# Optimization experiments

Hardware: AMD Instinct MI355X
Metric: run time of the kernel (lower is better)

The kernel has to match this reference:

```python
import jax, jax.numpy as jnp
import numpy as np

N_NODES = 100000
NEG_SLOPE = 0.2


def _gat_layer(x, src, dst, W, a_src, a_dst, b):
    """Single-head PyG-style GATConv (heads=1, concat, self-loops already in src/dst)."""
    h = x @ W                                   # [N, out]
    alpha_s = h @ a_src                          # [N]
    alpha_d = h @ a_dst                          # [N]
    e = jax.nn.leaky_relu(alpha_s[src] + alpha_d[dst], NEG_SLOPE)  # [E]
    # numerically stable softmax over incoming edges of each dst node
    m = jax.ops.segment_max(e, dst, num_segments=N_NODES)           # [N]
    ex = jnp.exp(e - m[dst])                                        # [E]
    denom = jax.ops.segment_sum(ex, dst, num_segments=N_NODES)      # [N]
    attn = ex / denom[dst]                                          # [E]
    out = jax.ops.segment_sum(h[src] * attn[:, None], dst, num_segments=N_NODES)
    return out + b


def setup_inputs() -> dict:
    key = jax.random.key(0)
    ks = jax.random.split(key, 16)
    F_IN, H1, H2 = 256, 64, 32
    E = 1600000
    x = jax.random.normal(ks[0], (N_NODES, F_IN), dtype=jnp.float32)
    edge_index = jax.random.randint(ks[1], (2, E), 0, N_NODES, dtype=jnp.int32)
    def glorot(k, shape):
        lim = float(np.sqrt(6.0 / (shape[0] + shape[-1])))
        return jax.random.uniform(k, shape, jnp.float32, -lim, lim)
    return {
        "x": x,
        "edge_index": edge_index,
        "W1": glorot(ks[2], (F_IN, H1)),
        "a_src1": glorot(ks[3], (H1,)),
        "a_dst1": glorot(ks[4], (H1,)),
        "b1": jnp.zeros((H1,), jnp.float32),
        "W2": glorot(ks[5], (H1, H2)),
        "a_src2": glorot(ks[6], (H2,)),
        "a_dst2": glorot(ks[7], (H2,)),
        "b2": jnp.zeros((H2,), jnp.float32),
        "Wfc": glorot(ks[8], (H2, 1)),
        "bfc": jnp.zeros((1,), jnp.float32),
    }


def reference(x, edge_index, W1, a_src1, a_dst1, b1, W2, a_src2, a_dst2, b2, Wfc, bfc):
    # add self loops (PyG GATConv default add_self_loops=True)
    loop = jnp.arange(N_NODES, dtype=edge_index.dtype)
    src = jnp.concatenate([edge_index[0], loop])
    dst = jnp.concatenate([edge_index[1], loop])
    h = jax.nn.relu(_gat_layer(x, src, dst, W1, a_src1, a_dst1, b1))
    h = jax.nn.relu(_gat_layer(h, src, dst, W2, a_src2, a_dst2, b2))
    return h @ Wfc + bfc  # [N, 1]
```

## Files before the change

kernel.cpp:

```cpp
#include <hip/hip_runtime.h>
#include <hip/hip_bf16.h>

#define NEG_SLOPE 0.2f
#define NINF (-1e30f)

#define BKT_BITS 7
#define BKT 128
#define PB 256

typedef __attribute__((ext_vector_type(8))) short s8v;
typedef __attribute__((ext_vector_type(4))) float f4v;

__device__ __forceinline__ unsigned short f2bf(float f) {
    unsigned u = __float_as_uint(f);
    u = (u + 0x7fffu + ((u >> 16) & 1u)) >> 16;
    return (unsigned short)u;
}
__device__ __forceinline__ float bf2f(unsigned short h) {
    return __uint_as_float(((unsigned)h) << 16);
}


__global__ __launch_bounds__(256) void hist_pb_k(
    const int* __restrict__ edst, int E, int Etot, int NBK, int EPB,
    int* __restrict__ counts)
{
    __shared__ int lh[1024];
    for (int i = threadIdx.x; i < NBK; i += 256) lh[i] = 0;
    __syncthreads();
    const int e0 = blockIdx.x * EPB;
    const int e1 = min(e0 + EPB, Etot);
    for (int i = e0 + threadIdx.x; i < e1; i += 256) {
        int d = (i < E) ? edst[i] : (i - E);
        atomicAdd(&lh[d >> BKT_BITS], 1);
    }
    __syncthreads();
    for (int b = threadIdx.x; b < NBK; b += 256)
        counts[b * PB + blockIdx.x] = lh[b];
}

__global__ __launch_bounds__(256) void scan_partial_k(
    const int* __restrict__ a, int L, int* __restrict__ partials)
{
    __shared__ int red[256];
    const int t = threadIdx.x;
    const int base = blockIdx.x * 1024 + t * 4;
    int sum = 0;
    #pragma unroll
    for (int k = 0; k < 4; ++k) {
        int i = base + k;
        if (i < L) sum += a[i];
    }
    red[t] = sum;
    __syncthreads();
    #pragma unroll
    for (int o = 128; o; o >>= 1) {
        if (t < o) red[t] += red[t + o];
        __syncthreads();
    }
    if (t == 0) partials[blockIdx.x] = red[0];
}

__global__ __launch_bounds__(256) void scan_partials_k(
    int* __restrict__ partials, int nb)
{
    __shared__ int sh[256];
    const int t = threadIdx.x;
    int v = (t < nb) ? partials[t] : 0;
    sh[t] = v;
    __syncthreads();
    #pragma unroll
    for (int o = 1; o < 256; o <<= 1) {
        int u = (t >= o) ? sh[t - o] : 0;
        __syncthreads();
        sh[t] += u;
        __syncthreads();
    }
    if (t < nb) partials[t] = sh[t] - v;
}

__global__ __launch_bounds__(256) void scan_final_k(
    int* __restrict__ a, const int* __restrict__ partials, int L)
{
    __shared__ int sh[256];
    const int t = threadIdx.x;
    const int base = blockIdx.x * 1024 + t * 4;
    int v[4];
    int sum = 0;
    #pragma unroll
    for (int k = 0; k < 4; ++k) {
        int i = base + k;
        v[k] = (i < L) ? a[i] : 0;
        sum += v[k];
    }
    sh[t] = sum;
    __syncthreads();
    #pragma unroll
    for (int o = 1; o < 256; o <<= 1) {
        int u = (t >= o) ? sh[t - o] : 0;
        __syncthreads();
        sh[t] += u;
        __syncthreads();
    }
    int run = sh[t] - sum + partials[blockIdx.x];
    #pragma unroll
    for (int k = 0; k < 4; ++k) {
        int i = base + k;
        if (i < L) a[i] = run;
        run += v[k];
    }
}

__global__ __launch_bounds__(256) void scatter_pb_k(
    const int* __restrict__ esrc, const int* __restrict__ edst,
    int E, int Etot, int NBK, int EPB,
    const int* __restrict__ cbase, unsigned* __restrict__ tmp)
{
    __shared__ int cur[1024];
    for (int b = threadIdx.x; b < NBK; b += 256)
        cur[b] = cbase[b * PB + blockIdx.x];
    __syncthreads();
    const int e0 = blockIdx.x * EPB;
    const int e1 = min(e0 + EPB, Etot);
    for (int i = e0 + threadIdx.x; i < e1; i += 256) {
        int d = (i < E) ? edst[i] : (i - E);
        int s = (i < E) ? esrc[i] : (i - E);
        int pos = atomicAdd(&cur[d >> BKT_BITS], 1);
        tmp[pos] = ((unsigned)s << BKT_BITS) | (unsigned)(d & (BKT - 1));
    }
}

__global__ __launch_bounds__(256) void bucket_finalize_k(
    const unsigned* __restrict__ tmp, const int* __restrict__ cbase,
    int N, int NBK, int Etot,
    int* __restrict__ rowptr, int* __restrict__ csr)
{
    __shared__ int cnt[BKT];
    __shared__ int off[BKT];
    const int b = blockIdx.x;
    const int t = threadIdx.x;
    const int start = cbase[b * PB];
    const int end = (b + 1 < NBK) ? cbase[(b + 1) * PB] : Etot;
    const int n0 = b << BKT_BITS;
    const int nn = min(BKT, N - n0);

    if (t < BKT) cnt[t] = 0;
    __syncthreads();
    for (int i = start + t; i < end; i += 256)
        atomicAdd(&cnt[tmp[i] & (BKT - 1)], 1);
    __syncthreads();
    if (t < BKT) off[t] = cnt[t];
    __syncthreads();
    #pragma unroll
    for (int o = 1; o < BKT; o <<= 1) {
        int u = (t >= o && t < BKT) ? off[t - o] : 0;
        __syncthreads();
        if (t < BKT) off[t] += u;
        __syncthreads();
    }
    if (t < BKT) {
        int ex = off[t] - cnt[t];
        if (t < nn) rowptr[n0 + t] = start + ex;
        cnt[t] = ex;
    }
    if (b == 0 && t == 0) rowptr[N] = Etot;
    __syncthreads();
    for (int i = start + t; i < end; i += 256) {
        unsigned w = tmp[i];
        int dl = w & (BKT - 1);
        int pos = atomicAdd(&cnt[dl], 1);
        csr[start + pos] = (int)(w >> BKT_BITS);
    }
}

__global__ __launch_bounds__(256) void prep_w_k(
    const float* __restrict__ W1, const float* __restrict__ W2,
    short* __restrict__ Wt1h, short* __restrict__ Wt1l,
    short* __restrict__ Wt2h, short* __restrict__ Wt2l)
{
    int t = blockIdx.x * 256 + threadIdx.x;
    if (t < 256 * 64) {
        int k = t >> 6, c = t & 63;
        float v = W1[t];
        unsigned short h = f2bf(v);
        unsigned short l = f2bf(v - bf2f(h));
        Wt1h[c * 256 + k] = (short)h;
        Wt1l[c * 256 + k] = (short)l;
    } else if (t < 256 * 64 + 64 * 32) {
        int e = t - 256 * 64;
        int k = e >> 5, c = e & 31;
        float v = W2[e];
        unsigned short h = f2bf(v);
        unsigned short l = f2bf(v - bf2f(h));
        Wt2h[c * 64 + k] = (short)h;
        Wt2l[c * 64 + k] = (short)l;
    }
}

template <int K, int M, bool RELU_BIAS>
__global__ __launch_bounds__(256) void gemm_mfma_k(
    const float* __restrict__ X,
    const short* __restrict__ Wth, const short* __restrict__ Wtl,
    const float* __restrict__ a_s, const float* __restrict__ a_d,
    const float* __restrict__ bias_in,
    unsigned short* __restrict__ Hb, float* __restrict__ AS, float* __restrict__ AD,
    int N)
{
    constexpr int NT = M / 16;
    constexpr int KS = K / 32;
    __shared__ short Xhi[64][40];
    __shared__ short Xlo[64][40];

    const int wave = threadIdx.x >> 6;
    const int lane = threadIdx.x & 63;
    const int lc = lane & 15;
    const int k8 = (lane >> 4) * 8;
    const int rb = blockIdx.x * 64;

    const int trow = threadIdx.x >> 2;
    const int tseg = (threadIdx.x & 3) * 8;

    f4v acc[NT];
    #pragma unroll
    for (int c = 0; c < NT; ++c) acc[c] = (f4v){0.f, 0.f, 0.f, 0.f};

    for (int ks = 0; ks < KS; ++ks) {
        int gr = rb + trow;
        float v[8];
        if (gr < N) {
            const float* src = X + (long)gr * K + ks * 32 + tseg;
            float4 v0 = *(const float4*)(src);
            float4 v1 = *(const float4*)(src + 4);
            v[0] = v0.x; v[1] = v0.y; v[2] = v0.z; v[3] = v0.w;
            v[4] = v1.x; v[5] = v1.y; v[6] = v1.z; v[7] = v1.w;
        } else {
            #pragma unroll
            for (int j = 0; j < 8; ++j) v[j] = 0.f;
        }
        if (RELU_BIAS) {
            #pragma unroll
            for (int j = 0; j < 8; ++j) {
                float w = v[j] + bias_in[ks * 32 + tseg + j];
                v[j] = w > 0.f ? w : 0.f;
            }
        }
        s8v hv, lv;
        #pragma unroll
        for (int j = 0; j < 8; ++j) {
            unsigned short h = f2bf(v[j]);
            hv[j] = (short)h;
            lv[j] = (short)f2bf(v[j] - bf2f(h));
        }
        *(s8v*)&Xhi[trow][tseg] = hv;
        *(s8v*)&Xlo[trow][tseg] = lv;
        __syncthreads();

        const int arow = wave * 16 + lc;
        s8v ah = *(const s8v*)&Xhi[arow][k8];
        s8v al = *(const s8v*)&Xlo[arow][k8];
        #pragma unroll
        for (int c = 0; c < NT; ++c) {
            const long wo = (long)(c * 16 + lc) * K + ks * 32 + k8;
            s8v bh = *(const s8v*)(Wth + wo);
            s8v bl = *(const s8v*)(Wtl + wo);
            acc[c] = __builtin_amdgcn_mfma_f32_16x16x32_bf16(ah, bh, acc[c], 0, 0, 0);
            acc[c] = __builtin_amdgcn_mfma_f32_16x16x32_bf16(al, bh, acc[c], 0, 0, 0);
            acc[c] = __builtin_amdgcn_mfma_f32_16x16x32_bf16(ah, bl, acc[c], 0, 0, 0);
        }
        __syncthreads();
    }

    float ps[4] = {0.f, 0.f, 0.f, 0.f}, pd[4] = {0.f, 0.f, 0.f, 0.f};
    #pragma unroll
    for (int c = 0; c < NT; ++c) {
        float asv = a_s[c * 16 + lc];
        float adv = a_d[c * 16 + lc];
        #pragma unroll
        for (int j = 0; j < 4; ++j) {
            float hval = acc[c][j];
            int grow = rb + wave * 16 + (lane >> 4) * 4 + j;
            if (grow < N) Hb[(long)grow * M + c * 16 + lc] = f2bf(hval);
            ps[j] = fmaf(hval, asv, ps[j]);
            pd[j] = fmaf(hval, adv, pd[j]);
        }
    }
    #pragma unroll
    for (int j = 0; j < 4; ++j) {
        #pragma unroll
        for (int o = 8; o >= 1; o >>= 1) {
            ps[j] += __shfl_xor(ps[j], o);
            pd[j] += __shfl_xor(pd[j], o);
        }
    }
    if (lc == 0) {
        #pragma unroll
        for (int j = 0; j < 4; ++j) {
            int grow = rb + wave * 16 + (lane >> 4) * 4 + j;
            if (grow < N) { AS[grow] = ps[j]; AD[grow] = pd[j]; }
        }
    }
}

template <int M>
__global__ __launch_bounds__(256) void agg_csr_k(
    const int* __restrict__ rowptr, const int* __restrict__ csr_src,
    const float* __restrict__ as_, const float* __restrict__ ad_,
    const unsigned short* __restrict__ H, float* __restrict__ OUT, int N)
{
    constexpr int LP = M / 2;
    constexpr int EH = 64 / LP;
    __shared__ float lw[4][64];
    __shared__ int   ls[4][64];
    const int wave = threadIdx.x >> 6;
    const int lane = threadIdx.x & 63;
    const int d = blockIdx.x * 4 + wave;
    if (d >= N) return;
    const int r0 = rowptr[d];
    const int deg = rowptr[d + 1] - r0;
    const float adv = ad_[d];

    const int f2 = (lane % LP) * 2;
    const int eh = lane / LP;

    float m = NINF, den = 0.0f, acc0 = 0.0f, acc1 = 0.0f;
    for (int base = 0; base < deg; base += 64) {
        int j = base + lane;
        int s = 0;
        float e = NINF;
        if (j < deg) {
            s = csr_src[r0 + j];
            e = as_[s] + adv;
            e = e > 0.0f ? e : NEG_SLOPE * e;
        }
        float cm = e;
        #pragma unroll
        for (int o = 32; o; o >>= 1) cm = fmaxf(cm, __shfl_xor(cm, o));
        if (cm > m) {
            float sc = __expf(m - cm);
            acc0 *= sc; acc1 *= sc; den *= sc; m = cm;
        }
        float w = __expf(e - m);
        float wsum = w;
        #pragma unroll
        for (int o = 32; o; o >>= 1) wsum += __shfl_xor(wsum, o);
        den += wsum;
        lw[wave][lane] = w;
        ls[wave][lane] = s;
        int cnt = min(64, deg - base);
        #pragma unroll 4
        for (int jj = 0; jj < cnt; jj += EH) {
            int je = jj + eh;
            float wj = (je < cnt) ? lw[wave][je] : 0.0f;
            int   sj = (je < cnt) ? ls[wave][je] : 0;
            unsigned hv = *(const unsigned*)&H[(long)sj * M + f2];
            acc0 = fmaf(wj, bf2f((unsigned short)(hv & 0xffffu)), acc0);
            acc1 = fmaf(wj, bf2f((unsigned short)(hv >> 16)), acc1);
        }
    }
    #pragma unroll
    for (int o = LP; o < 64; o <<= 1) {
        acc0 += __shfl_xor(acc0, o);
        acc1 += __shfl_xor(acc1, o);
    }
    if (lane < LP) {
        float inv = 1.0f / den;
        *(float2*)&OUT[(long)d * M + f2] = make_float2(acc0 * inv, acc1 * inv);
    }
}

__global__ __launch_bounds__(256) void fc_out_k(
    const float* __restrict__ H2, const float* __restrict__ b2,
    const float* __restrict__ Wfc, const float* __restrict__ bfc,
    float* __restrict__ out, int N)
{
    int t = blockIdx.x * 256 + threadIdx.x;
    int n = t >> 5;
    int fidx = t & 31;
    if (n >= N) return;
    float v = H2[(long)n * 32 + fidx] + b2[fidx];
    v = v > 0.0f ? v : 0.0f;
    v *= Wfc[fidx];
    #pragma unroll
    for (int o = 16; o >= 1; o >>= 1) v += __shfl_xor(v, o, 32);
    if (fidx == 0) out[n] = v + bfc[0];
}

extern "C" void kernel_launch(void* const* d_in, const int* in_sizes, int n_in,
                              void* d_out, int out_size, void* d_ws, size_t ws_size,
                              hipStream_t stream) {
    const float* x      = (const float*)d_in[0];
    const int*   eidx   = (const int*)d_in[1];
    const float* W1     = (const float*)d_in[2];
    const float* a_src1 = (const float*)d_in[3];
    const float* a_dst1 = (const float*)d_in[4];
    const float* b1     = (const float*)d_in[5];
    const float* W2     = (const float*)d_in[6];
    const float* a_src2 = (const float*)d_in[7];
    const float* a_dst2 = (const float*)d_in[8];
    const float* b2     = (const float*)d_in[9];
    const float* Wfc    = (const float*)d_in[10];
    const float* bfc    = (const float*)d_in[11];
    float* out = (float*)d_out;

    const int N = in_sizes[0] / 256;
    const int E = in_sizes[1] / 2;
    const int Etot = E + N;
    const int* esrc = eidx;
    const int* edst = eidx + E;
    const int NBK = (N + BKT - 1) >> BKT_BITS;
    const int EPB = (Etot + PB - 1) / PB;
    const int L   = NBK * PB;

    char* cur = (char*)d_ws;
    auto alloc = [&](size_t bytes) -> void* {
        void* r = (void*)cur;
        cur += (bytes + 255) & ~(size_t)255;
        return r;
    };
    int* rowptr   = (int*)alloc((size_t)(N + 1) * 4);
    int* counts   = (int*)alloc((size_t)L * 4);
    int* partials = (int*)alloc(1024);
    unsigned* tmp = (unsigned*)alloc((size_t)Etot * 4);
    int* csr      = (int*)alloc((size_t)Etot * 4);
    float* as1    = (float*)alloc((size_t)N * 4);
    float* ad1    = (float*)alloc((size_t)N * 4);
    float* as2    = (float*)alloc((size_t)N * 4);
    float* ad2    = (float*)alloc((size_t)N * 4);
    short* Wt1h   = (short*)alloc(16384 * 2);
    short* Wt1l   = (short*)alloc(16384 * 2);
    short* Wt2h   = (short*)alloc(2048 * 2);
    short* Wt2l   = (short*)alloc(2048 * 2);
    unsigned short* h1b = (unsigned short*)alloc((size_t)N * 64 * 2);
    unsigned short* h2b = (unsigned short*)alloc((size_t)N * 32 * 2);
    float* h1out  = (float*)alloc((size_t)N * 64 * 4);
    float* h2out  = (float*)alloc((size_t)N * 32 * 4);

    prep_w_k<<<72, 256, 0, stream>>>(W1, W2, Wt1h, Wt1l, Wt2h, Wt2l);
    {
        int nb1 = (L + 1023) / 1024;
        hist_pb_k<<<PB, 256, 0, stream>>>(edst, E, Etot, NBK, EPB, counts);
        scan_partial_k<<<nb1, 256, 0, stream>>>(counts, L, partials);
        scan_partials_k<<<1, 256, 0, stream>>>(partials, nb1);
        scan_final_k<<<nb1, 256, 0, stream>>>(counts, partials, L);
        scatter_pb_k<<<PB, 256, 0, stream>>>(esrc, edst, E, Etot, NBK, EPB, counts, tmp);
        bucket_finalize_k<<<NBK, 256, 0, stream>>>(tmp, counts, N, NBK, Etot, rowptr, csr);
    }

    const int gemmBlocks = (N + 63) / 64;
    const int aggBlocks  = (N + 3) / 4;

    gemm_mfma_k<256, 64, false><<<gemmBlocks, 256, 0, stream>>>(
        x, Wt1h, Wt1l, a_src1, a_dst1, nullptr, h1b, as1, ad1, N);
    agg_csr_k<64><<<aggBlocks, 256, 0, stream>>>(
        rowptr, csr, as1, ad1, h1b, h1out, N);

    gemm_mfma_k<64, 32, true><<<gemmBlocks, 256, 0, stream>>>(
        h1out, Wt2h, Wt2l, a_src2, a_dst2, b1, h2b, as2, ad2, N);
    agg_csr_k<32><<<aggBlocks, 256, 0, stream>>>(
        rowptr, csr, as2, ad2, h2b, h2out, N);

    {
        int blocks = (int)(((long)N * 32 + 255) / 256);
        fc_out_k<<<blocks, 256, 0, stream>>>(h2out, b2, Wfc, bfc, out, N);
    }
}
```

Before: 394.0 us.

## Double-buffer GEMM LDS tiles and fuse layer-2 aggregation with final FC

The MFMA GEMM now uses two LDS buffers and prefetches the next K-slice of X into registers while the current slice is multiplied. This removes one barrier per iteration and hides global load latency. Separately, the second-layer aggregation is fused with bias, ReLU and the final linear projection, so the N×32 fp32 intermediate is never written or re-read and one kernel launch is dropped. The cost is doubled LDS use and more live registers in the GEMM.

```diff
diff --git a/kernel.cpp b/kernel.cpp
--- a/kernel.cpp
+++ b/kernel.cpp
@@ -208,8 +208,8 @@
 {
     constexpr int NT = M / 16;
     constexpr int KS = K / 32;
-    __shared__ short Xhi[64][40];
-    __shared__ short Xlo[64][40];
+    __shared__ short Xhi[2][64][40];
+    __shared__ short Xlo[2][64][40];
 
     const int wave = threadIdx.x >> 6;
     const int lane = threadIdx.x & 63;
@@ -219,18 +219,19 @@
 
     const int trow = threadIdx.x >> 2;
     const int tseg = (threadIdx.x & 3) * 8;
+    const int gr = rb + trow;
+    const bool rok = gr < N;
+    const float* xrow = X + (long)gr * K + tseg;
 
     f4v acc[NT];
     #pragma unroll
     for (int c = 0; c < NT; ++c) acc[c] = (f4v){0.f, 0.f, 0.f, 0.f};
 
-    for (int ks = 0; ks < KS; ++ks) {
-        int gr = rb + trow;
-        float v[8];
-        if (gr < N) {
-            const float* src = X + (long)gr * K + ks * 32 + tseg;
-            float4 v0 = *(const float4*)(src);
-            float4 v1 = *(const float4*)(src + 4);
+    float v[8];
+    {
+        if (rok) {
+            float4 v0 = *(const float4*)(xrow);
+            float4 v1 = *(const float4*)(xrow + 4);
             v[0] = v0.x; v[1] = v0.y; v[2] = v0.z; v[3] = v0.w;
             v[4] = v1.x; v[5] = v1.y; v[6] = v1.z; v[7] = v1.w;
         } else {
@@ -240,7 +241,7 @@
         if (RELU_BIAS) {
             #pragma unroll
             for (int j = 0; j < 8; ++j) {
-                float w = v[j] + bias_in[ks * 32 + tseg + j];
+                float w = v[j] + bias_in[tseg + j];
                 v[j] = w > 0.f ? w : 0.f;
             }
         }
@@ -251,13 +252,28 @@
             hv[j] = (short)h;
             lv[j] = (short)f2bf(v[j] - bf2f(h));
         }
-        *(s8v*)&Xhi[trow][tseg] = hv;
-        *(s8v*)&Xlo[trow][tseg] = lv;
+        *(s8v*)&Xhi[0][trow][tseg] = hv;
+        *(s8v*)&Xlo[0][trow][tseg] = lv;
+    }
+
+    for (int ks = 0; ks < KS; ++ks) {
+        float vn[8];
+        if (ks + 1 < KS) {
+            if (rok) {
+                float4 v0 = *(const float4*)(xrow + (ks + 1) * 32);
+                float4 v1 = *(const float4*)(xrow + (ks + 1) * 32 + 4);
+                vn[0] = v0.x; vn[1] = v0.y; vn[2] = v0.z; vn[3] = v0.w;
+                vn[4] = v1.x; vn[5] = v1.y; vn[6] = v1.z; vn[7] = v1.w;
+            } else {
+                #pragma unroll
+                for (int j = 0; j < 8; ++j) vn[j] = 0.f;
+            }
+        }
         __syncthreads();
 
         const int arow = wave * 16 + lc;
-        s8v ah = *(const s8v*)&Xhi[arow][k8];
-        s8v al = *(const s8v*)&Xlo[arow][k8];
+        s8v ah = *(const s8v*)&Xhi[ks & 1][arow][k8];
+        s8v al = *(const s8v*)&Xlo[ks & 1][arow][k8];
         #pragma unroll
         for (int c = 0; c < NT; ++c) {
             const long wo = (long)(c * 16 + lc) * K + ks * 32 + k8;
@@ -267,7 +283,25 @@
             acc[c] = __builtin_amdgcn_mfma_f32_16x16x32_bf16(al, bh, acc[c], 0, 0, 0);
             acc[c] = __builtin_amdgcn_mfma_f32_16x16x32_bf16(ah, bl, acc[c], 0, 0, 0);
         }
-        __syncthreads();
+
+        if (ks + 1 < KS) {
+            if (RELU_BIAS) {
+                #pragma unroll
+                for (int j = 0; j < 8; ++j) {
+                    float w = vn[j] + bias_in[(ks + 1) * 32 + tseg + j];
+                    vn[j] = w > 0.f ? w : 0.f;
+                }
+            }
+            s8v hv, lv;
+            #pragma unroll
+            for (int j = 0; j < 8; ++j) {
+                unsigned short h = f2bf(vn[j]);
+                hv[j] = (short)h;
+                lv[j] = (short)f2bf(vn[j] - bf2f(h));
+            }
+            *(s8v*)&Xhi[(ks + 1) & 1][trow][tseg] = hv;
+            *(s8v*)&Xlo[(ks + 1) & 1][trow][tseg] = lv;
+        }
     }
 
     float ps[4] = {0.f, 0.f, 0.f, 0.f}, pd[4] = {0.f, 0.f, 0.f, 0.f};
@@ -301,14 +335,12 @@
     }
 }
 
-template <int M>
 __global__ __launch_bounds__(256) void agg_csr_k(
     const int* __restrict__ rowptr, const int* __restrict__ csr_src,
     const float* __restrict__ as_, const float* __restrict__ ad_,
     const unsigned short* __restrict__ H, float* __restrict__ OUT, int N)
 {
-    constexpr int LP = M / 2;
-    constexpr int EH = 64 / LP;
+    constexpr int M = 64, LP = 32, EH = 2;
     __shared__ float lw[4][64];
     __shared__ int   ls[4][64];
     const int wave = threadIdx.x >> 6;
@@ -368,21 +400,77 @@
     }
 }
 
-__global__ __launch_bounds__(256) void fc_out_k(
-    const float* __restrict__ H2, const float* __restrict__ b2,
-    const float* __restrict__ Wfc, const float* __restrict__ bfc,
+__global__ __launch_bounds__(256) void agg_fc_k(
+    const int* __restrict__ rowptr, const int* __restrict__ csr_src,
+    const float* __restrict__ as_, const float* __restrict__ ad_,
+    const unsigned short* __restrict__ H,
+    const float* __restrict__ b2, const float* __restrict__ Wfc,
+    const float* __restrict__ bfc,
     float* __restrict__ out, int N)
 {
-    int t = blockIdx.x * 256 + threadIdx.x;
-    int n = t >> 5;
-    int fidx = t & 31;
-    if (n >= N) return;
-    float v = H2[(long)n * 32 + fidx] + b2[fidx];
-    v = v > 0.0f ? v : 0.0f;
-    v *= Wfc[fidx];
-    #pragma unroll
-    for (int o = 16; o >= 1; o >>= 1) v += __shfl_xor(v, o, 32);
-    if (fidx == 0) out[n] = v + bfc[0];
+    constexpr int M = 32, LP = 16, EH = 4;
+    __shared__ float lw[4][64];
+    __shared__ int   ls[4][64];
+    const int wave = threadIdx.x >> 6;
+    const int lane = threadIdx.x & 63;
+    const int d = blockIdx.x * 4 + wave;
+    if (d >= N) return;
+    const int r0 = rowptr[d];
+    const int deg = rowptr[d + 1] - r0;
+    const float adv = ad_[d];
+
+    const int f2 = (lane % LP) * 2;
+    const int eh = lane / LP;
+
+    float m = NINF, den = 0.0f, acc0 = 0.0f, acc1 = 0.0f;
+    for (int base = 0; base < deg; base += 64) {
+        int j = base + lane;
+        int s = 0;
+        float e = NINF;
+        if (j < deg) {
+            s = csr_src[r0 + j];
+            e = as_[s] + adv;
+            e = e > 0.0f ? e : NEG_SLOPE * e;
+        }
+        float cm = e;
+        #pragma unroll
+        for (int o = 32; o; o >>= 1) cm = fmaxf(cm, __shfl_xor(cm, o));
+        if (cm > m) {
+            float sc = __expf(m - cm);
+            acc0 *= sc; acc1 *= sc; den *= sc; m = cm;
+        }
+        float w = __expf(e - m);
+        float wsum = w;
+        #pragma unroll
+        for (int o = 32; o; o >>= 1) wsum += __shfl_xor(wsum, o);
+        den += wsum;
+        lw[wave][lane] = w;
+        ls[wave][lane] = s;
+        int cnt = min(64, deg - base);
+        #pragma unroll 4
+        for (int jj = 0; jj < cnt; jj += EH) {
+            int je = jj + eh;
+            float wj = (je < cnt) ? lw[wave][je] : 0.0f;
+            int   sj = (je < cnt) ? ls[wave][je] : 0;
+            unsigned hv = *(const unsigned*)&H[(long)sj * M + f2];
+            acc0 = fmaf(wj, bf2f((unsigned short)(hv & 0xffffu)), acc0);
+            acc1 = fmaf(wj, bf2f((unsigned short)(hv >> 16)), acc1);
+        }
+    }
+    #pragma unroll
+    for (int o = LP; o < 64; o <<= 1) {
+        acc0 += __shfl_xor(acc0, o);
+        acc1 += __shfl_xor(acc1, o);
+    }
+    float inv = 1.0f / den;
+    float h0 = acc0 * inv + b2[f2];
+    float h1 = acc1 * inv + b2[f2 + 1];
+    h0 = h0 > 0.f ? h0 : 0.f;
+    h1 = h1 > 0.f ? h1 : 0.f;
+    float p = h0 * Wfc[f2] + h1 * Wfc[f2 + 1];
+    #pragma unroll
+    for (int o = 8; o >= 1; o >>= 1) p += __shfl_xor(p, o);
+    if (lane == 0) out[d] = p + bfc[0];
 }
 
 extern "C" void kernel_launch(void* const* d_in, const int* in_sizes, int n_in,
@@ -433,7 +521,6 @@
     unsigned short* h1b = (unsigned short*)alloc((size_t)N * 64 * 2);
     unsigned short* h2b = (unsigned short*)alloc((size_t)N * 32 * 2);
     float* h1out  = (float*)alloc((size_t)N * 64 * 4);
-    float* h2out  = (float*)alloc((size_t)N * 32 * 4);
 
     prep_w_k<<<72, 256, 0, stream>>>(W1, W2, Wt1h, Wt1l, Wt2h, Wt2l);
     {
@@ -451,16 +538,12 @@
 
     gemm_mfma_k<256, 64, false><<<gemmBlocks, 256, 0, stream>>>(
         x, Wt1h, Wt1l, a_src1, a_dst1, nullptr, h1b, as1, ad1, N);
-    agg_csr_k<64><<<aggBlocks, 256, 0, stream>>>(
+    agg_csr_k<<<aggBlocks, 256, 0, stream>>>(
         rowptr, csr, as1, ad1, h1b, h1out, N);
 
     gemm_mfma_k<64, 32, true><<<gemmBlocks, 256, 0, stream>>>(
         h1out, Wt2h, Wt2l, a_src2, a_dst2, b1, h2b, as2, ad2, N);
-    agg_csr_k<32><<<aggBlocks, 256, 0, stream>>>(
-        rowptr, csr, as2, ad2, h2b, h2out, N);
-
-    {
-        int blocks = (int)(((long)N * 32 + 255) / 256);
-        fc_out_k<<<blocks, 256, 0, stream>>>(h2out, b2, Wfc, bfc, out, N);
-    }
-}
+
+    agg_fc_k<<<aggBlocks, 256, 0, stream>>>(
+        rowptr, csr, as2, ad2, h2b, b2, Wfc, bfc, out, N);
+}
```

After: 391.8 us. No clear change (-0.6%).
